# Kernel optimization log

Measured on AMD Instinct MI355X. Metric: run time of the kernel, lower is better.

Reference implementation:

```python
import jax, jax.numpy as jnp
import numpy as np

B, S, D = 2, 1024, 2048
H, HKV, HD = 16, 8, 128
F, E, R = 5632, 8, 16
EPS = 1e-5
SCALE = 2.0  # lora_alpha / r = 32 / 16


def _rope_tables():
    pos = jnp.arange(S, dtype=jnp.float32)
    inv = 1.0 / (10000.0 ** (jnp.arange(0, HD, 2, dtype=jnp.float32) / HD))
    ang = pos[:, None] * inv[None, :]  # [S, HD/2]
    return jnp.cos(ang), jnp.sin(ang)


def setup_inputs() -> dict:
    key = jax.random.key(0)
    ks = jax.random.split(key, 18)
    p = lambda k, shp: jax.random.normal(k, shp, dtype=jnp.float32) * 0.02
    cos, sin = _rope_tables()
    return {
        'data': jax.random.normal(ks[0], (B, S, D), dtype=jnp.float32),
        'mask': jnp.zeros((1, 1, S, S), dtype=jnp.float32),
        'rope_cos': cos,
        'rope_sin': sin,
        'attn_norm_w': jnp.ones((D,), jnp.float32),
        'ffn_norm_w': jnp.ones((D,), jnp.float32),
        'wq': p(ks[1], (D, D)),
        'wk': p(ks[2], (HKV * HD, D)),
        'wv': p(ks[3], (HKV * HD, D)),
        'wo': p(ks[4], (D, D)),
        'gate_w': p(ks[5], (E, D)),
        'w1': p(ks[6], (F, D)),
        'w2': p(ks[7], (D, F)),
        'w3': p(ks[8], (F, D)),
        'w1_a': p(ks[9], (E, R, D)),
        'w1_b': p(ks[10], (E, F, R)),
        'w3_a': p(ks[11], (E, R, D)),
        'w3_b': p(ks[12], (E, F, R)),
        'w2_a': p(ks[13], (E, R, F)),
        'w2_b': p(ks[14], (E, D, R)),
    }


def _rmsnorm(x, w):
    v = jnp.mean(x.astype(jnp.float32) ** 2, axis=-1, keepdims=True)
    return (x * jax.lax.rsqrt(v + EPS)).astype(x.dtype) * w


def _rope(x, cos, sin):
    # x: [B,S,h,HD]; interleaved-pair rotation (llama apply_rotary_emb)
    x1, x2 = x[..., 0::2], x[..., 1::2]
    c, s = cos[None, :, None, :], sin[None, :, None, :]
    o1 = x1 * c - x2 * s
    o2 = x1 * s + x2 * c
    return jnp.stack([o1, o2], axis=-1).reshape(x.shape)


def reference(data, mask, rope_cos, rope_sin, attn_norm_w, ffn_norm_w,
              wq, wk, wv, wo, gate_w, w1, w2, w3,
              w1_a, w1_b, w3_a, w3_b, w2_a, w2_b):
    # ---- attention block ----
    xn = _rmsnorm(data, attn_norm_w)
    q = (xn @ wq.T).reshape(B, S, H, HD)
    k = (xn @ wk.T).reshape(B, S, HKV, HD)
    v = (xn @ wv.T).reshape(B, S, HKV, HD)
    q = _rope(q, rope_cos, rope_sin)
    k = _rope(k, rope_cos, rope_sin)
    k = jnp.repeat(k, H // HKV, axis=2)  # repeat_kv
    v = jnp.repeat(v, H // HKV, axis=2)
    scores = jnp.einsum('bqhd,bkhd->bhqk', q, k) / np.float32(np.sqrt(HD)) + mask
    probs = jax.nn.softmax(scores, axis=-1)
    attn = jnp.einsum('bhqk,bkhd->bqhd', probs, v).reshape(B, S, H * HD)
    data = data + attn @ wo.T
    # ---- MoE block ----
    sn = _rmsnorm(data, ffn_norm_w)
    logits = sn @ gate_w.T  # [B,S,E]
    # NOTE: source uses F.softmax(..., dim=1) -> softmax over SEQ axis, replicated faithfully
    rw = jax.nn.softmax(logits.astype(jnp.float32), axis=1)
    rw, sel = jax.lax.top_k(rw, 2)  # over experts (last axis)
    rw = rw / jnp.sum(rw, axis=-1, keepdims=True)
    c1 = sn @ w1.T  # [B,S,F]
    c3 = sn @ w3.T
    acc = jnp.zeros_like(data)
    for e in range(E):  # dense per-expert loop, as in source
        h1 = c1 + ((sn @ w1_a[e].T) @ w1_b[e].T) * SCALE
        h3 = c3 + ((sn @ w3_a[e].T) @ w3_b[e].T) * SCALE
        sr = jax.nn.silu(h1) * h3
        h = sr @ w2.T + ((sr @ w2_a[e].T) @ w2_b[e].T) * SCALE
        ew = jnp.sum(rw * (sel == e), axis=-1, keepdims=True).astype(h.dtype)
        acc = acc + h * ew
    return data + acc
```

## Files before the change

kernel.cpp:

```cpp
#include <hip/hip_runtime.h>
#include <hip/hip_bf16.h>
#include <stdint.h>

#define DEVI __device__ __forceinline__

typedef __attribute__((ext_vector_type(8))) short short8;
typedef __attribute__((ext_vector_type(4))) short short4b;
typedef __attribute__((ext_vector_type(4))) float f32x4;

constexpr int Bb  = 2, Ss = 1024, Dd = 2048, Hh = 16, HKVv = 8, HDd = 128;
constexpr int Ff  = 5632, Ee = 8, Rr = 16;
constexpr int Tt  = Bb * Ss;
constexpr int M2  = 2 * Tt;
constexpr int NKV = HKVv * HDd;
constexpr int NQKV = Dd + 2 * NKV;

DEVI unsigned short f2bf(float f) {
  union { float f; unsigned u; } x; x.f = f;
  unsigned r = (x.u + 0x7FFFu + ((x.u >> 16) & 1u)) >> 16;
  return (unsigned short)r;
}
DEVI float bf2f(unsigned short h) {
  union { unsigned u; float f; } x; x.u = ((unsigned)h) << 16; return x.f;
}
DEVI float wsum64(float v) {
  #pragma unroll
  for (int d = 1; d < 64; d <<= 1) v += __shfl_xor(v, d, 64);
  return v;
}
DEVI float wsum16(float v) {
  v += __shfl_xor(v, 1, 64); v += __shfl_xor(v, 2, 64);
  v += __shfl_xor(v, 4, 64); v += __shfl_xor(v, 8, 64);
  return v;
}
DEVI float wmax16(float v) {
  v = fmaxf(v, __shfl_xor(v, 1, 64)); v = fmaxf(v, __shfl_xor(v, 2, 64));
  v = fmaxf(v, __shfl_xor(v, 4, 64)); v = fmaxf(v, __shfl_xor(v, 8, 64));
  return v;
}
typedef __attribute__((address_space(1))) void gvoid;
typedef __attribute__((address_space(3))) void lvoid;
DEVI void gl_lds16(const void* g, void* l) {
  __builtin_amdgcn_global_load_lds((gvoid*)g, (lvoid*)l, 16, 0, 0);
}
DEVI unsigned ldsoff(const void* p) {
  return (unsigned)(uintptr_t)(lvoid*)p;
}
DEVI f32x4 mfma16x16(short8 a, short8 b, f32x4 c) {
  return __builtin_amdgcn_mfma_f32_16x16x32_bf16(a, b, c, 0, 0, 0);
}

__global__ __launch_bounds__(256) void cast_w(const float* __restrict__ in,
                                              unsigned short* __restrict__ out, int n) {
  int i = (blockIdx.x * 256 + threadIdx.x) * 8;
  if (i >= n) return;
  const float4* p = (const float4*)(in + i);
  float4 a = p[0], b = p[1];
  float v[8] = {a.x,a.y,a.z,a.w,b.x,b.y,b.z,b.w};
  short8 o;
  #pragma unroll
  for (int j = 0; j < 8; ++j) o[j] = (short)f2bf(v[j]);
  *(short8*)(out + i) = o;
}
__global__ __launch_bounds__(256) void cast_split_w(const float* __restrict__ in,
                                                    unsigned short* __restrict__ oh,
                                                    unsigned short* __restrict__ ol, int n) {
  int i = (blockIdx.x * 256 + threadIdx.x) * 8;
  if (i >= n) return;
  const float4* p = (const float4*)(in + i);
  float4 a = p[0], b = p[1];
  float v[8] = {a.x,a.y,a.z,a.w,b.x,b.y,b.z,b.w};
  short8 h, l;
  #pragma unroll
  for (int j = 0; j < 8; ++j) {
    unsigned short hb = f2bf(v[j]);
    h[j] = (short)hb;
    l[j] = (short)f2bf(v[j] - bf2f(hb));
  }
  *(short8*)(oh + i) = h;
  *(short8*)(ol + i) = l;
}

__global__ __launch_bounds__(256) void rmsnorm_k(const float* __restrict__ x,
                                                 const float* __restrict__ w,
                                                 unsigned short* __restrict__ out) {
  int row = blockIdx.x, tid = threadIdx.x;
  const float* xr = x + (size_t)row * Dd;
  const float4* p4 = (const float4*)(xr + tid * 8);
  float4 a = p4[0], b = p4[1];
  float v[8] = {a.x,a.y,a.z,a.w,b.x,b.y,b.z,b.w};
  float ss = 0.f;
  #pragma unroll
  for (int j = 0; j < 8; ++j) ss += v[j] * v[j];
  ss = wsum64(ss);
  __shared__ float red[4];
  int wv_ = tid >> 6, l = tid & 63;
  if (l == 0) red[wv_] = ss;
  __syncthreads();
  float tot = red[0] + red[1] + red[2] + red[3];
  float rstd = rsqrtf(tot * (1.0f / Dd) + 1e-5f);
  const float* wr = w + tid * 8;
  short8 o;
  #pragma unroll
  for (int j = 0; j < 8; ++j) o[j] = (short)f2bf(v[j] * rstd * wr[j]);
  *(short8*)(out + (size_t)row * Dd + tid * 8) = o;
}

__global__ __launch_bounds__(256) void rmsnorm_split_k(const float* __restrict__ x,
                                                       const float* __restrict__ w,
                                                       unsigned short* __restrict__ outh,
                                                       unsigned short* __restrict__ outl) {
  int row = blockIdx.x, tid = threadIdx.x;
  const float* xr = x + (size_t)row * Dd;
  const float4* p4 = (const float4*)(xr + tid * 8);
  float4 a = p4[0], b = p4[1];
  float v[8] = {a.x,a.y,a.z,a.w,b.x,b.y,b.z,b.w};
  float ss = 0.f;
  #pragma unroll
  for (int j = 0; j < 8; ++j) ss += v[j] * v[j];
  ss = wsum64(ss);
  __shared__ float red[4];
  int wv_ = tid >> 6, l = tid & 63;
  if (l == 0) red[wv_] = ss;
  __syncthreads();
  float tot = red[0] + red[1] + red[2] + red[3];
  float rstd = rsqrtf(tot * (1.0f / Dd) + 1e-5f);
  const float* wr = w + tid * 8;
  short8 oh, ol;
  #pragma unroll
  for (int j = 0; j < 8; ++j) {
    float val = v[j] * rstd * wr[j];
    unsigned short hb = f2bf(val);
    oh[j] = (short)hb;
    ol[j] = (short)f2bf(val - bf2f(hb));
  }
  *(short8*)(outh + (size_t)row * Dd + tid * 8) = oh;
  *(short8*)(outl + (size_t)row * Dd + tid * 8) = ol;
}

template <int MODE>
__global__ __launch_bounds__(256) void gemm_bt64_db(const unsigned short* __restrict__ A,
                                                    const unsigned short* __restrict__ Bw,
                                                    void* __restrict__ Cout,
                                                    int M, int N, int K, int gx) {
  __shared__ __align__(16) unsigned short As[2][128 * 64];
  __shared__ __align__(16) unsigned short Bs[2][128 * 64];
  int tid = threadIdx.x;
  int w = tid >> 6, l = tid & 63;
  int lr = l & 15, lg = l >> 4;
  int cpx = (int)gridDim.x >> 3;
  int bid = blockIdx.x;
  int swz = (bid & 7) * cpx + (bid >> 3);
  int bx = swz % gx, by = swz / gx;
  int m0 = by * 128, n0 = bx * 128;
  int wr = (w >> 1) * 64, wc = (w & 1) * 64;
  f32x4 acc[4][4];
  #pragma unroll
  for (int i = 0; i < 4; ++i)
    #pragma unroll
    for (int j = 0; j < 4; ++j) acc[i][j] = (f32x4){0.f, 0.f, 0.f, 0.f};

  int srow = w * 32 + (l >> 3);
  int schunk = (l & 7) ^ (l >> 3);
  const unsigned short* ga = A  + (size_t)(m0 + srow) * K + schunk * 8;
  const unsigned short* gb = Bw + (size_t)(n0 + srow) * K + schunk * 8;

  auto STAGE = [&](int b, int k0) {
    #pragma unroll
    for (int c = 0; c < 4; ++c) {
      gl_lds16(ga + k0 + (size_t)(c * 8) * K, As[b] + w * 2048 + c * 512);
      gl_lds16(gb + k0 + (size_t)(c * 8) * K, Bs[b] + w * 2048 + c * 512);
    }
  };
  auto COMP = [&](int b) {
    const unsigned short* Ab = As[b];
    const unsigned short* Bb = Bs[b];
    #pragma unroll
    for (int kk = 0; kk < 2; ++kk) {
      short8 af[4], bfr[4];
      #pragma unroll
      for (int i = 0; i < 4; ++i)
        af[i]  = *(const short8*)(Ab + (wr + i * 16 + lr) * 64 + (((kk * 4 + lg) ^ (lr & 7)) * 8));
      #pragma unroll
      for (int j = 0; j < 4; ++j)
        bfr[j] = *(const short8*)(Bb + (wc + j * 16 + lr) * 64 + (((kk * 4 + lg) ^ (lr & 7)) * 8));
      #pragma unroll
      for (int i = 0; i < 4; ++i)
        #pragma unroll
        for (int j = 0; j < 4; ++j) acc[i][j] = mfma16x16(af[i], bfr[j], acc[i][j]);
    }
  };

  int nk = K >> 6;
  STAGE(0, 0);
  __syncthreads();
  int cur = 0;
  for (int kt = 0; kt < nk - 1; ++kt) {
    STAGE(cur ^ 1, (kt + 1) << 6);
    COMP(cur);
    __syncthreads();
    cur ^= 1;
  }
  COMP(cur);

  #pragma unroll
  for (int i = 0; i < 4; ++i)
    #pragma unroll
    for (int j = 0; j < 4; ++j) {
      int m = m0 + wr + i * 16 + lg * 4;
      int n = n0 + wc + j * 16 + lr;
      #pragma unroll
      for (int r = 0; r < 4; ++r) {
        float vv = acc[i][j][r];
        size_t o = (size_t)(m + r) * N + n;
        if (MODE == 0) ((unsigned short*)Cout)[o] = f2bf(vv);
        else           ((float*)Cout)[o] = vv;
      }
    }
}

template <int MODE>
__global__ __launch_bounds__(256) void gemm3_bt(const unsigned short* __restrict__ Ah,
                                                const unsigned short* __restrict__ Al,
                                                const unsigned short* __restrict__ Bh1,
                                                const unsigned short* __restrict__ Bl1,
                                                const unsigned short* __restrict__ Bh2,
                                                const unsigned short* __restrict__ Bl2,
                                                const unsigned short* __restrict__ Bh3,
                                                const unsigned short* __restrict__ Bl3,
                                                int nsplit1, int nsplit2,
                                                void* __restrict__ C0,
                                                const float* __restrict__ resid,
                                                int M, int N, int K, int gx) {
  __shared__ __align__(16) unsigned short Ash[128 * 32];
  __shared__ __align__(16) unsigned short Asl[128 * 32];
  __shared__ __align__(16) unsigned short Bsh[128 * 32];
  __shared__ __align__(16) unsigned short Bsl[128 * 32];
  int tid = threadIdx.x;
  int w = tid >> 6, l = tid & 63;
  int lr = l & 15, lg = l >> 4;
  int cpx = (int)gridDim.x >> 3;
  int bid = blockIdx.x;
  int swz = (bid & 7) * cpx + (bid >> 3);
  int bx = swz % gx, by = swz / gx;
  int m0 = by * 128, n0 = bx * 128;
  int wr = (w >> 1) * 64, wc = (w & 1) * 64;

  const unsigned short* Bh; const unsigned short* Bl; int nb;
  if (n0 < nsplit1)      { Bh = Bh1; Bl = Bl1; nb = n0; }
  else if (n0 < nsplit2) { Bh = Bh2; Bl = Bl2; nb = n0 - nsplit1; }
  else                   { Bh = Bh3; Bl = Bl3; nb = n0 - nsplit2; }

  f32x4 acc[4][4];
  #pragma unroll
  for (int i = 0; i < 4; ++i)
    #pragma unroll
    for (int j = 0; j < 4; ++j) acc[i][j] = (f32x4){0.f, 0.f, 0.f, 0.f};

  int srow = w * 32 + (l >> 2);
  int scol = ((l & 3) ^ ((l >> 3) & 3)) * 8;
  const unsigned short* gah = Ah + (size_t)(m0 + srow) * K + scol;
  const unsigned short* gal = Al + (size_t)(m0 + srow) * K + scol;
  const unsigned short* gbh = Bh + (size_t)(nb + srow) * K + scol;
  const unsigned short* gbl = Bl + (size_t)(nb + srow) * K + scol;
  unsigned short* lAh = Ash + w * 1024;
  unsigned short* lAl = Asl + w * 1024;
  unsigned short* lBh = Bsh + w * 1024;
  unsigned short* lBl = Bsl + w * 1024;

  for (int k0 = 0; k0 < K; k0 += 32) {
    gl_lds16(gah + k0, lAh); gl_lds16(gah + (size_t)16 * K + k0, lAh + 512);
    gl_lds16(gal + k0, lAl); gl_lds16(gal + (size_t)16 * K + k0, lAl + 512);
    gl_lds16(gbh + k0, lBh); gl_lds16(gbh + (size_t)16 * K + k0, lBh + 512);
    gl_lds16(gbl + k0, lBl); gl_lds16(gbl + (size_t)16 * K + k0, lBl + 512);
    __syncthreads();
    int rc = (lg ^ ((lr >> 1) & 3)) * 8;
    short8 afh[4], afl[4], bfh[4], bfl[4];
    #pragma unroll
    for (int i = 0; i < 4; ++i) {
      afh[i] = *(const short8*)(Ash + (wr + i * 16 + lr) * 32 + rc);
      afl[i] = *(const short8*)(Asl + (wr + i * 16 + lr) * 32 + rc);
    }
    #pragma unroll
    for (int j = 0; j < 4; ++j) {
      bfh[j] = *(const short8*)(Bsh + (wc + j * 16 + lr) * 32 + rc);
      bfl[j] = *(const short8*)(Bsl + (wc + j * 16 + lr) * 32 + rc);
    }
    #pragma unroll
    for (int i = 0; i < 4; ++i)
      #pragma unroll
      for (int j = 0; j < 4; ++j) {
        acc[i][j] = mfma16x16(afh[i], bfh[j], acc[i][j]);
        acc[i][j] = mfma16x16(afh[i], bfl[j], acc[i][j]);
        acc[i][j] = mfma16x16(afl[i], bfh[j], acc[i][j]);
      }
    __syncthreads();
  }
  #pragma unroll
  for (int i = 0; i < 4; ++i)
    #pragma unroll
    for (int j = 0; j < 4; ++j) {
      int m = m0 + wr + i * 16 + lg * 4;
      int n = n0 + wc + j * 16 + lr;
      #pragma unroll
      for (int r = 0; r < 4; ++r) {
        float vv = acc[i][j][r];
        size_t o = (size_t)(m + r) * N + n;
        if (MODE == 1) ((float*)C0)[o] = vv;
        else           ((float*)C0)[o] = vv + resid[o];
      }
    }
}

__global__ __launch_bounds__(128) void vsplit_k(const float* __restrict__ qkv,
                                                unsigned short* __restrict__ vh,
                                                unsigned short* __restrict__ vl) {
  int row = blockIdx.x;
  int bas = threadIdx.x * 8;
  const float4* p = (const float4*)(qkv + (size_t)row * NQKV + Dd + NKV + bas);
  float4 a = p[0], b = p[1];
  float v[8] = {a.x,a.y,a.z,a.w,b.x,b.y,b.z,b.w};
  short8 h, l;
  #pragma unroll
  for (int j = 0; j < 8; ++j) {
    unsigned short hb = f2bf(v[j]);
    h[j] = (short)hb;
    l[j] = (short)f2bf(v[j] - bf2f(hb));
  }
  size_t o = (size_t)row * NKV + bas;
  *(short8*)(vh + o) = h;
  *(short8*)(vl + o) = l;
}

__global__ void rope_split_k(const float* __restrict__ x, int xstride,
                             const float* __restrict__ cs, const float* __restrict__ sn,
                             unsigned short* __restrict__ oh, unsigned short* __restrict__ ol,
                             int nh) {
  int row = blockIdx.x;
  int s = row & (Ss - 1);
  int nelem = nh * HDd;
  int bas = threadIdx.x * 8;
  if (bas >= nelem) return;
  const float4* px = (const float4*)(x + (size_t)row * xstride + bas);
  float4 a = px[0], b = px[1];
  float vv[8] = {a.x,a.y,a.z,a.w,b.x,b.y,b.z,b.w};
  int d = bas & (HDd - 1);
  const float* cr = cs + s * 64 + (d >> 1);
  const float* sr = sn + s * 64 + (d >> 1);
  short8 hs, ls;
  #pragma unroll
  for (int p = 0; p < 4; ++p) {
    float x1 = vv[2 * p], x2 = vv[2 * p + 1];
    float c = cr[p], si = sr[p];
    float o1 = x1 * c - x2 * si;
    float o2 = x1 * si + x2 * c;
    unsigned short h1 = f2bf(o1), h2 = f2bf(o2);
    hs[2 * p] = (short)h1;      hs[2 * p + 1] = (short)h2;
    ls[2 * p] = (short)f2bf(o1 - bf2f(h1));
    ls[2 * p + 1] = (short)f2bf(o2 - bf2f(h2));
  }
  size_t o = (size_t)row * nelem + bas;
  *(short8*)(oh + o) = hs;
  *(short8*)(ol + o) = ls;
}

__global__ __launch_bounds__(256) void attn3_k(const unsigned short* __restrict__ qh,
                                               const unsigned short* __restrict__ ql,
                                               const unsigned short* __restrict__ kh,
                                               const unsigned short* __restrict__ kl,
                                               const unsigned short* __restrict__ vh,
                                               const unsigned short* __restrict__ vl,
                                               const float* __restrict__ mask,
                                               unsigned short* __restrict__ aoh,
                                               unsigned short* __restrict__ aol) {
  __shared__ __align__(16) unsigned short Ksh[32 * 128], Ksl[32 * 128];
  __shared__ __align__(16) unsigned short VTh[8 * 528], VTl[8 * 528];
  __shared__ __align__(16) unsigned short Plh[4 * 16 * 40], Pll[4 * 16 * 40];
  int tid = threadIdx.x, w = tid >> 6, l = tid & 63;
  int lr = l & 15, lg = l >> 4;
  int b = blockIdx.y >> 4, h = blockIdx.y & 15, hk = h >> 1;
  int q0 = blockIdx.x * 64 + w * 16;

  short8 qfh[4], qfl[4];
  {
    size_t qoff = ((size_t)((b * Ss + q0 + lr) * Hh + h)) * HDd;
    #pragma unroll
    for (int ds = 0; ds < 4; ++ds) {
      qfh[ds] = *(const short8*)(qh + qoff + ds * 32 + lg * 8);
      qfl[ds] = *(const short8*)(ql + qoff + ds * 32 + lg * 8);
    }
  }

  float mreg[4] = {-1e30f, -1e30f, -1e30f, -1e30f};
  float lreg[4] = {0.f, 0.f, 0.f, 0.f};
  f32x4 oacc[8];
  #pragma unroll
  for (int db = 0; db < 8; ++db) oacc[db] = (f32x4){0.f, 0.f, 0.f, 0.f};

  const float sc = 0.08838834764831845f;
  size_t kvbase = ((size_t)(b * Ss) * HKVv + hk) * HDd;
  const unsigned short* kb_h = kh + kvbase;
  const unsigned short* kb_l = kl + kvbase;
  const unsigned short* vb_h = vh + kvbase;
  const unsigned short* vb_l = vl + kvbase;

  int kc1 = (lr ^ lg) * 8;
  int kc2 = (lr ^ (lg + 4)) * 8;
  int vrow_a = w * 8 + ((l & 7) >> 1);
  int vchunk = ((l >> 3) * 2 + (l & 1)) * 8;
  unsigned short* vh1 = VTh + (2 * w) * 528;
  unsigned short* vh2 = VTh + (2 * w + 1) * 528;
  unsigned short* vl1 = VTl + (2 * w) * 528;
  unsigned short* vl2 = VTl + (2 * w + 1) * 528;
  unsigned vtbh = ldsoff(VTh) + (unsigned)lr * 8u;
  unsigned vtbl = ldsoff(VTl) + (unsigned)lr * 8u;

  for (int kv0 = 0; kv0 < Ss; kv0 += 32) {
    int r1 = kv0 + w * 8 + lg;
    gl_lds16(kb_h + (size_t)r1 * NKV + kc1,       Ksh + w * 1024);
    gl_lds16(kb_h + (size_t)(r1 + 4) * NKV + kc2, Ksh + w * 1024 + 512);
    gl_lds16(kb_l + (size_t)r1 * NKV + kc1,       Ksl + w * 1024);
    gl_lds16(kb_l + (size_t)(r1 + 4) * NKV + kc2, Ksl + w * 1024 + 512);
    int vr0 = kv0 + vrow_a;
    gl_lds16(vb_h + (size_t)vr0 * NKV + vchunk,       vh1);
    gl_lds16(vb_h + (size_t)(vr0 + 4) * NKV + vchunk, vh2);
    gl_lds16(vb_l + (size_t)vr0 * NKV + vchunk,       vl1);
    gl_lds16(vb_l + (size_t)(vr0 + 4) * NKV + vchunk, vl2);
    __syncthreads();

    f32x4 s0 = (f32x4){0.f,0.f,0.f,0.f}, s1 = (f32x4){0.f,0.f,0.f,0.f};
    #pragma unroll
    for (int ds = 0; ds < 4; ++ds) {
      int kcol = ((ds * 4 + lg) ^ (lr & 7)) * 8;
      short8 kh0 = *(const short8*)(Ksh + lr * 128 + kcol);
      short8 kh1 = *(const short8*)(Ksh + (16 + lr) * 128 + kcol);
      short8 kl0 = *(const short8*)(Ksl + lr * 128 + kcol);
      short8 kl1 = *(const short8*)(Ksl + (16 + lr) * 128 + kcol);
      s0 = mfma16x16(qfh[ds], kh0, s0);
      s0 = mfma16x16(qfh[ds], kl0, s0);
      s0 = mfma16x16(qfl[ds], kh0, s0);
      s1 = mfma16x16(qfh[ds], kh1, s1);
      s1 = mfma16x16(qfh[ds], kl1, s1);
      s1 = mfma16x16(qfl[ds], kh1, s1);
    }
    const float* mrow = mask + (size_t)(q0 + lg * 4) * Ss + kv0 + lr;
    #pragma unroll
    for (int r = 0; r < 4; ++r) {
      float a0 = s0[r] * sc + mrow[(size_t)r * Ss];
      float a1 = s1[r] * sc + mrow[(size_t)r * Ss + 16];
      float t = wmax16(fmaxf(a0, a1));
      float mn = fmaxf(mreg[r], t);
      float resc = __expf(mreg[r] - mn);
      mreg[r] = mn;
      float e0 = __expf(a0 - mn), e1 = __expf(a1 - mn);
      float ps = wsum16(e0 + e1);
      lreg[r] = lreg[r] * resc + ps;
      #pragma unroll
      for (int db = 0; db < 8; ++db) oacc[db][r] *= resc;
      unsigned short h0 = f2bf(e0), h1 = f2bf(e1);
      unsigned short* prowh = Plh + (w * 16 + lg * 4 + r) * 40;
      unsigned short* prowl = Pll + (w * 16 + lg * 4 + r) * 40;
      prowh[lr] = h0;            prowh[16 + lr] = h1;
      prowl[lr] = f2bf(e0 - bf2f(h0));
      prowl[16 + lr] = f2bf(e1 - bf2f(h1));
    }
    asm volatile("" ::: "memory");
    short8 pfh = *(const short8*)(Plh + (w * 16 + lr) * 40 + lg * 8);
    short8 pfl = *(const short8*)(Pll + (w * 16 + lr) * 40 + lg * 8);

    short4b v4[16];
    #pragma unroll
    for (int db = 0; db < 8; ++db) {
      #pragma unroll
      for (int t = 0; t < 2; ++t) {
        unsigned off = vtbh + (unsigned)((lg * 2 + t) * 1056 + db * 128);
        asm volatile("ds_read_b64_tr_b16 %0, %1" : "=v"(v4[db * 2 + t]) : "v"(off));
      }
    }
    asm volatile("s_waitcnt lgkmcnt(0)" ::: "memory");
    __builtin_amdgcn_sched_barrier(0);
    #pragma unroll
    for (int db = 0; db < 8; ++db) {
      short8 vf;
      vf[0] = v4[db*2][0]; vf[1] = v4[db*2][1]; vf[2] = v4[db*2][2]; vf[3] = v4[db*2][3];
      vf[4] = v4[db*2+1][0]; vf[5] = v4[db*2+1][1]; vf[6] = v4[db*2+1][2]; vf[7] = v4[db*2+1][3];
      oacc[db] = mfma16x16(pfh, vf, oacc[db]);
      oacc[db] = mfma16x16(pfl, vf, oacc[db]);
    }
    #pragma unroll
    for (int db = 0; db < 8; ++db) {
      #pragma unroll
      for (int t = 0; t < 2; ++t) {
        unsigned off = vtbl + (unsigned)((lg * 2 + t) * 1056 + db * 128);
        asm volatile("ds_read_b64_tr_b16 %0, %1" : "=v"(v4[db * 2 + t]) : "v"(off));
      }
    }
    asm volatile("s_waitcnt lgkmcnt(0)" ::: "memory");
    __builtin_amdgcn_sched_barrier(0);
    #pragma unroll
    for (int db = 0; db < 8; ++db) {
      short8 vf;
      vf[0] = v4[db*2][0]; vf[1] = v4[db*2][1]; vf[2] = v4[db*2][2]; vf[3] = v4[db*2][3];
      vf[4] = v4[db*2+1][0]; vf[5] = v4[db*2+1][1]; vf[6] = v4[db*2+1][2]; vf[7] = v4[db*2+1][3];
      oacc[db] = mfma16x16(pfh, vf, oacc[db]);
    }
    __syncthreads();
  }
  float inv[4];
  #pragma unroll
  for (int r = 0; r < 4; ++r) inv[r] = 1.0f / lreg[r];
  size_t obase = ((size_t)((b * Ss + q0 + lg * 4) * Hh + h)) * HDd + lr;
  #pragma unroll
  for (int db = 0; db < 8; ++db)
    #pragma unroll
    for (int r = 0; r < 4; ++r) {
      float val = oacc[db][r] * inv[r];
      unsigned short hb = f2bf(val);
      size_t o = obase + (size_t)r * Hh * HDd + db * 16;
      aoh[o] = hb;
      aol[o] = f2bf(val - bf2f(hb));
    }
}

__global__ __launch_bounds__(256) void router_logits(const float* __restrict__ x2,
                                                     const float* __restrict__ fnw,
                                                     const float* __restrict__ gw,
                                                     float* __restrict__ logits) {
  int wid = (blockIdx.x * 256 + threadIdx.x) >> 6;
  int l = threadIdx.x & 63;
  if (wid >= Tt) return;
  const float* row = x2 + (size_t)wid * Dd;
  float xs[32]; float ss = 0.f;
  #pragma unroll
  for (int c = 0; c < 32; ++c) { float t = row[c * 64 + l]; xs[c] = t; ss += t * t; }
  ss = wsum64(ss);
  float rstd = rsqrtf(ss * (1.0f / Dd) + 1e-5f);
  #pragma unroll
  for (int c = 0; c < 32; ++c) xs[c] *= rstd * fnw[c * 64 + l];
  for (int e = 0; e < 8; ++e) {
    float a = 0.f;
    #pragma unroll
    for (int c = 0; c < 32; ++c) a += xs[c] * gw[(size_t)e * Dd + c * 64 + l];
    a = wsum64(a);
    if (l == 0) logits[wid * 8 + e] = a;
  }
}
__global__ __launch_bounds__(256) void router_colstats(const float* __restrict__ logits,
                                                       float* __restrict__ mz) {
  int b = blockIdx.x >> 3, e = blockIdx.x & 7;
  int tid = threadIdx.x, wv_ = tid >> 6, l = tid & 63;
  __shared__ float red[4];
  float mx = -1e30f;
  for (int s = tid; s < Ss; s += 256) mx = fmaxf(mx, logits[(size_t)(b * Ss + s) * 8 + e]);
  #pragma unroll
  for (int d = 1; d < 64; d <<= 1) mx = fmaxf(mx, __shfl_xor(mx, d, 64));
  if (l == 0) red[wv_] = mx;
  __syncthreads();
  mx = fmaxf(fmaxf(red[0], red[1]), fmaxf(red[2], red[3]));
  __syncthreads();
  float z = 0.f;
  for (int s = tid; s < Ss; s += 256) z += expf(logits[(size_t)(b * Ss + s) * 8 + e] - mx);
  z = wsum64(z);
  if (l == 0) red[wv_] = z;
  __syncthreads();
  if (tid == 0) {
    mz[(b * 8 + e) * 2] = mx;
    mz[(b * 8 + e) * 2 + 1] = red[0] + red[1] + red[2] + red[3];
  }
}
__global__ __launch_bounds__(256) void router_select(const float* __restrict__ logits,
                                                     const float* __restrict__ mz,
                                                     int* __restrict__ sel,
                                                     float* __restrict__ ewt) {
  int t = blockIdx.x * 256 + threadIdx.x;
  if (t >= Tt) return;
  int b = t >> 10;
  float rw[8];
  #pragma unroll
  for (int e = 0; e < 8; ++e)
    rw[e] = expf(logits[(size_t)t * 8 + e] - mz[(b * 8 + e) * 2]) / mz[(b * 8 + e) * 2 + 1];
  int i0 = 0; float b0 = rw[0];
  #pragma unroll
  for (int e = 1; e < 8; ++e) if (rw[e] > b0) { b0 = rw[e]; i0 = e; }
  int i1 = -1; float b1 = -1.f;
  #pragma unroll
  for (int e = 0; e < 8; ++e) if (e != i0 && rw[e] > b1) { b1 = rw[e]; i1 = e; }
  float s = b0 + b1;
  sel[2 * t] = i0; sel[2 * t + 1] = i1;
  ewt[2 * t] = b0 / s; ewt[2 * t + 1] = b1 / s;
}
__global__ void zero_cnt_k(int* cnt) { if (threadIdx.x < 8) cnt[threadIdx.x] = 0; }
__global__ void gather_k(const int* __restrict__ sel, int* cnt, int* list) {
  int i = blockIdx.x * 256 + threadIdx.x;
  if (i >= M2) return;
  int e = sel[i];
  int pos = atomicAdd(cnt + e, 1);
  list[e * Tt + pos] = i;
}

__global__ __launch_bounds__(256) void lora_up_k(const unsigned short* __restrict__ snb,
                                                 const int* __restrict__ sel,
                                                 const float* __restrict__ w1a,
                                                 const float* __restrict__ w3a,
                                                 float* __restrict__ t1, float* __restrict__ t3) {
  int i = (blockIdx.x * 256 + threadIdx.x) >> 6;
  int l = threadIdx.x & 63;
  if (i >= M2) return;
  int t = i >> 1, e = sel[i];
  const unsigned short* row = snb + (size_t)t * Dd;
  const float* wa1 = w1a + (size_t)e * Rr * Dd;
  const float* wa3 = w3a + (size_t)e * Rr * Dd;
  float a1[16], a3[16];
  #pragma unroll
  for (int r = 0; r < 16; ++r) { a1[r] = 0.f; a3[r] = 0.f; }
  for (int c0 = 0; c0 < 32; c0 += 8) {
    float xs[8];
    #pragma unroll
    for (int c = 0; c < 8; ++c) xs[c] = bf2f(row[(c0 + c) * 64 + l]);
    #pragma unroll
    for (int r = 0; r < 16; ++r) {
      float s1 = a1[r], s3 = a3[r];
      #pragma unroll
      for (int c = 0; c < 8; ++c) {
        s1 += xs[c] * wa1[(size_t)r * Dd + (c0 + c) * 64 + l];
        s3 += xs[c] * wa3[(size_t)r * Dd + (c0 + c) * 64 + l];
      }
      a1[r] = s1; a3[r] = s3;
    }
  }
  #pragma unroll
  for (int r = 0; r < 16; ++r) { a1[r] = wsum64(a1[r]); a3[r] = wsum64(a3[r]); }
  if (l == 0) {
    #pragma unroll
    for (int r = 0; r < 16; ++r) { t1[i * 16 + r] = a1[r]; t3[i * 16 + r] = a3[r]; }
  }
}

__global__ __launch_bounds__(256) void expert_sr_k(const unsigned short* __restrict__ c1,
                                                   const unsigned short* __restrict__ c3,
                                                   const float* __restrict__ t1,
                                                   const float* __restrict__ t3,
                                                   const float* __restrict__ w1b,
                                                   const float* __restrict__ w3b,
                                                   const int* __restrict__ cnt,
                                                   const int* __restrict__ list,
                                                   unsigned short* __restrict__ sr) {
  int e = blockIdx.y;
  int f = blockIdx.x * 256 + threadIdx.x;
  __shared__ float W1[16 * 256], W3[16 * 256];
  #pragma unroll
  for (int r = 0; r < 16; ++r) {
    W1[r * 256 + threadIdx.x] = 2.0f * w1b[((size_t)e * Ff + f) * 16 + r];
    W3[r * 256 + threadIdx.x] = 2.0f * w3b[((size_t)e * Ff + f) * 16 + r];
  }
  __syncthreads();
  int n = cnt[e];
  int chunk = (n + 3) >> 2;
  int pbeg = blockIdx.z * chunk;
  int pend = min(n, pbeg + chunk);
  for (int p = pbeg; p < pend; ++p) {
    int i = list[e * Tt + p];
    int t = i >> 1;
    const float* u1 = t1 + (size_t)i * 16;
    const float* u3 = t3 + (size_t)i * 16;
    float l1 = 0.f, l3 = 0.f;
    #pragma unroll
    for (int r = 0; r < 16; ++r) {
      l1 += u1[r] * W1[r * 256 + threadIdx.x];
      l3 += u3[r] * W3[r * 256 + threadIdx.x];
    }
    float h1 = bf2f(c1[(size_t)t * Ff + f]) + l1;
    float h3 = bf2f(c3[(size_t)t * Ff + f]) + l3;
    float sv = (h1 / (1.f + __expf(-h1))) * h3;
    sr[(size_t)i * Ff + f] = f2bf(sv);
  }
}

__global__ __launch_bounds__(256) void lora_down_k(const unsigned short* __restrict__ sr,
                                                   const int* __restrict__ sel,
                                                   const float* __restrict__ w2a,
                                                   float* __restrict__ t2) {
  int i = (blockIdx.x * 256 + threadIdx.x) >> 6;
  int l = threadIdx.x & 63;
  if (i >= M2) return;
  int e = sel[i];
  const unsigned short* row = sr + (size_t)i * Ff;
  const float* wa = w2a + (size_t)e * Rr * Ff;
  float acc[16];
  #pragma unroll
  for (int r = 0; r < 16; ++r) acc[r] = 0.f;
  for (int c0 = 0; c0 < 88; c0 += 11) {
    float xs[11];
    #pragma unroll
    for (int c = 0; c < 11; ++c) xs[c] = bf2f(row[(c0 + c) * 64 + l]);
    #pragma unroll
    for (int r = 0; r < 16; ++r) {
      float a = acc[r];
      #pragma unroll
      for (int c = 0; c < 11; ++c) a += xs[c] * wa[(size_t)r * Ff + (c0 + c) * 64 + l];
      acc[r] = a;
    }
  }
  #pragma unroll
  for (int r = 0; r < 16; ++r) acc[r] = wsum64(acc[r]);
  if (l == 0) {
    #pragma unroll
    for (int r = 0; r < 16; ++r) t2[i * 16 + r] = acc[r];
  }
}

__global__ __launch_bounds__(256) void combine_k(const float* __restrict__ hb,
                                                 const float* __restrict__ t2,
                                                 const int* __restrict__ sel,
                                                 const float* __restrict__ ewt,
                                                 const float* __restrict__ w2b,
                                                 float* __restrict__ out) {
  int t = blockIdx.x;
  int d0 = threadIdx.x * 8;
  int e0 = sel[2 * t], e1 = sel[2 * t + 1];
  float a0 = ewt[2 * t], a1 = ewt[2 * t + 1];
  float uu0[16], uu1[16];
  const float* u0 = t2 + (size_t)(2 * t) * 16;
  const float* u1 = t2 + (size_t)(2 * t + 1) * 16;
  #pragma unroll
  for (int r = 0; r < 16; ++r) { uu0[r] = u0[r]; uu1[r] = u1[r]; }
  const float* wb0 = w2b + (size_t)e0 * Dd * 16;
  const float* wb1 = w2b + (size_t)e1 * Dd * 16;
  const float* h0 = hb + (size_t)(2 * t) * Dd;
  const float* h1 = hb + (size_t)(2 * t + 1) * Dd;
  float* orow = out + (size_t)t * Dd;
  #pragma unroll
  for (int dd = 0; dd < 8; ++dd) {
    int d = d0 + dd;
    float l0 = 0.f, l1v = 0.f;
    #pragma unroll
    for (int r = 0; r < 16; ++r) {
      l0  += uu0[r] * wb0[(size_t)d * 16 + r];
      l1v += uu1[r] * wb1[(size_t)d * 16 + r];
    }
    orow[d] += a0 * (h0[d] + 2.f * l0) + a1 * (h1[d] + 2.f * l1v);
  }
}

extern "C" void kernel_launch(void* const* d_in, const int* in_sizes, int n_in,
                              void* d_out, int out_size, void* d_ws, size_t ws_size,
                              hipStream_t stream) {
  const float* data  = (const float*)d_in[0];
  const float* mask  = (const float*)d_in[1];
  const float* ropec = (const float*)d_in[2];
  const float* ropes = (const float*)d_in[3];
  const float* anw   = (const float*)d_in[4];
  const float* fnw   = (const float*)d_in[5];
  const float* wq_f  = (const float*)d_in[6];
  const float* wk_f  = (const float*)d_in[7];
  const float* wv_f  = (const float*)d_in[8];
  const float* wo_f  = (const float*)d_in[9];
  const float* gate  = (const float*)d_in[10];
  const float* w1_f  = (const float*)d_in[11];
  const float* w2_f  = (const float*)d_in[12];
  const float* w3_f  = (const float*)d_in[13];
  const float* w1a   = (const float*)d_in[14];
  const float* w1bl  = (const float*)d_in[15];
  const float* w3a   = (const float*)d_in[16];
  const float* w3bl  = (const float*)d_in[17];
  const float* w2a   = (const float*)d_in[18];
  const float* w2bl  = (const float*)d_in[19];
  float* out = (float*)d_out;

  char* base = (char*)d_ws;
  size_t off = 0;
  auto take = [&](size_t bytes) -> char* {
    char* r = base + off;
    off += (bytes + 255) & ~(size_t)255;
    return r;
  };
  unsigned short* wqh = (unsigned short*)take((size_t)Dd * Dd * 2);
  unsigned short* wql = (unsigned short*)take((size_t)Dd * Dd * 2);
  unsigned short* wkh = (unsigned short*)take((size_t)NKV * Dd * 2);
  unsigned short* wkl = (unsigned short*)take((size_t)NKV * Dd * 2);
  unsigned short* wvh = (unsigned short*)take((size_t)NKV * Dd * 2);
  unsigned short* wvl = (unsigned short*)take((size_t)NKV * Dd * 2);
  unsigned short* woh = (unsigned short*)take((size_t)Dd * Dd * 2);
  unsigned short* wol = (unsigned short*)take((size_t)Dd * Dd * 2);
  unsigned short* w1bf = (unsigned short*)take((size_t)Ff * Dd * 2);
  unsigned short* w2bf = (unsigned short*)take((size_t)Dd * Ff * 2);
  unsigned short* w3bf = (unsigned short*)take((size_t)Ff * Dd * 2);
  unsigned short* xh = (unsigned short*)take((size_t)Tt * Dd * 2);
  unsigned short* xl = (unsigned short*)take((size_t)Tt * Dd * 2);
  unsigned short* qhB = (unsigned short*)take((size_t)Tt * Dd * 2);
  unsigned short* qlB = (unsigned short*)take((size_t)Tt * Dd * 2);
  unsigned short* khB = (unsigned short*)take((size_t)Tt * NKV * 2);
  unsigned short* klB = (unsigned short*)take((size_t)Tt * NKV * 2);
  unsigned short* vhB = (unsigned short*)take((size_t)Tt * NKV * 2);
  unsigned short* vlB = (unsigned short*)take((size_t)Tt * NKV * 2);
  unsigned short* srb = (unsigned short*)take((size_t)M2 * Ff * 2);
  float* hb = (float*)take((size_t)M2 * Dd * 4);
  float* t1b = (float*)take((size_t)M2 * 16 * 4);
  float* t3b = (float*)take((size_t)M2 * 16 * 4);
  float* t2b = (float*)take((size_t)M2 * 16 * 4);
  int*   selb = (int*)take((size_t)M2 * 4);
  float* ewtb = (float*)take((size_t)M2 * 4);
  float* logitsb = (float*)take((size_t)Tt * 8 * 4);
  float* mzb = (float*)take((size_t)16 * 2 * 4);
  int*   cntb = (int*)take(8 * 4);
  int*   listb = (int*)take((size_t)8 * Tt * 4);
  if (off > ws_size) return;

  float* qkv = (float*)hb;
  unsigned short* aoh = xh;
  unsigned short* aol = xl;
  unsigned short* snb = qhB;
  unsigned short* c1b = qlB;
  unsigned short* c3b = wqh;

  cast_split_w<<<2048, 256, 0, stream>>>(wq_f, wqh, wql, Dd * Dd);
  cast_split_w<<<1024, 256, 0, stream>>>(wk_f, wkh, wkl, NKV * Dd);
  cast_split_w<<<1024, 256, 0, stream>>>(wv_f, wvh, wvl, NKV * Dd);
  cast_split_w<<<2048, 256, 0, stream>>>(wo_f, woh, wol, Dd * Dd);
  cast_w<<<5632, 256, 0, stream>>>(w1_f, w1bf, Ff * Dd);
  cast_w<<<5632, 256, 0, stream>>>(w2_f, w2bf, Dd * Ff);
  cast_w<<<5632, 256, 0, stream>>>(w3_f, w3bf, Ff * Dd);

  rmsnorm_split_k<<<Tt, 256, 0, stream>>>(data, anw, xh, xl);
  gemm3_bt<1><<<512, 256, 0, stream>>>(xh, xl, wqh, wql, wkh, wkl, wvh, wvl,
                                       Dd, Dd + NKV, qkv, nullptr, Tt, NQKV, Dd, 32);
  vsplit_k<<<Tt, 128, 0, stream>>>(qkv, vhB, vlB);
  rope_split_k<<<Tt, 256, 0, stream>>>(qkv, NQKV, ropec, ropes, qhB, qlB, Hh);
  rope_split_k<<<Tt, 128, 0, stream>>>(qkv + Dd, NQKV, ropec, ropes, khB, klB, HKVv);
  attn3_k<<<dim3(16, 32), 256, 0, stream>>>(qhB, qlB, khB, klB, vhB, vlB, mask, aoh, aol);
  gemm3_bt<2><<<256, 256, 0, stream>>>(aoh, aol, woh, wol, woh, wol, woh, wol,
                                       Dd, Dd, d_out, data, Tt, Dd, Dd, 16);

  rmsnorm_k<<<Tt, 256, 0, stream>>>(out, fnw, snb);
  router_logits<<<512, 256, 0, stream>>>(out, fnw, gate, logitsb);
  router_colstats<<<16, 256, 0, stream>>>(logitsb, mzb);
  router_select<<<8, 256, 0, stream>>>(logitsb, mzb, selb, ewtb);
  zero_cnt_k<<<1, 64, 0, stream>>>(cntb);
  gather_k<<<16, 256, 0, stream>>>(selb, cntb, listb);
  gemm_bt64_db<0><<<704, 256, 0, stream>>>(snb, w1bf, c1b, Tt, Ff, Dd, 44);
  gemm_bt64_db<0><<<704, 256, 0, stream>>>(snb, w3bf, c3b, Tt, Ff, Dd, 44);
  lora_up_k<<<1024, 256, 0, stream>>>(snb, selb, w1a, w3a, t1b, t3b);
  expert_sr_k<<<dim3(22, 8, 4), 256, 0, stream>>>(c1b, c3b, t1b, t3b, w1bl, w3bl, cntb, listb, srb);
  lora_down_k<<<1024, 256, 0, stream>>>(srb, selb, w2a, t2b);
  gemm_bt64_db<1><<<512, 256, 0, stream>>>(srb, w2bf, hb, M2, Dd, Ff, 16);
  combine_k<<<Tt, 256, 0, stream>>>(hb, t2b, selb, ewtb, w2bl, out);
}
```

Before: 1.031 ms.

## Merge w1/w3 GEMMs, split-K the w2 GEMM, single-buffer LDS

The w1 and w3 weights are cast into one concatenated matrix, so c1 and c3 come from a single GEMM launch over 2F output columns. The w2 down-projection GEMM is split into two K halves writing separate fp32 partial buffers, which combine_k sums, doubling the block count. The GEMM kernel drops LDS double-buffering for a single buffer with two barriers per K step, halving shared memory and possibly raising occupancy at the cost of load/compute overlap. expert_sr_k splits its token range across twice as many z-blocks.

After: 1.024 ms. No clear change (-0.8%).

```diff
diff --git a/kernel.cpp b/kernel.cpp
--- a/kernel.cpp
+++ b/kernel.cpp
@@ -14,6 +14,7 @@
 constexpr int M2  = 2 * Tt;
 constexpr int NKV = HKVv * HDd;
 constexpr int NQKV = Dd + 2 * NKV;
+constexpr int F2  = 2 * Ff;
 
 DEVI unsigned short f2bf(float f) {
   union { float f; unsigned u; } x; x.f = f;
@@ -139,12 +140,13 @@
 }
 
 template <int MODE>
-__global__ __launch_bounds__(256) void gemm_bt64_db(const unsigned short* __restrict__ A,
+__global__ __launch_bounds__(256) void gemm_bt64_v2(const unsigned short* __restrict__ A,
                                                     const unsigned short* __restrict__ Bw,
-                                                    void* __restrict__ Cout,
-                                                    int M, int N, int K, int gx) {
-  __shared__ __align__(16) unsigned short As[2][128 * 64];
-  __shared__ __align__(16) unsigned short Bs[2][128 * 64];
+                                                    void* __restrict__ C0,
+                                                    void* __restrict__ C1,
+                                                    int M, int N, int Kext, int ld, int gx) {
+  __shared__ __align__(16) unsigned short As[128 * 64];
+  __shared__ __align__(16) unsigned short Bs[128 * 64];
   int tid = threadIdx.x;
   int w = tid >> 6, l = tid & 63;
   int lr = l & 15, lg = l >> 4;
@@ -152,7 +154,11 @@
   int bid = blockIdx.x;
   int swz = (bid & 7) * cpx + (bid >> 3);
   int bx = swz % gx, by = swz / gx;
+  int mtiles = M >> 7;
+  int ks = 0;
+  if (by >= mtiles) { ks = 1; by -= mtiles; }
   int m0 = by * 128, n0 = bx * 128;
+  int koff = ks * Kext;
   int wr = (w >> 1) * 64, wc = (w & 1) * 64;
   f32x4 acc[4][4];
   #pragma unroll
@@ -162,47 +168,35 @@
 
   int srow = w * 32 + (l >> 3);
   int schunk = (l & 7) ^ (l >> 3);
-  const unsigned short* ga = A  + (size_t)(m0 + srow) * K + schunk * 8;
-  const unsigned short* gb = Bw + (size_t)(n0 + srow) * K + schunk * 8;
-
-  auto STAGE = [&](int b, int k0) {
+  const unsigned short* ga = A  + (size_t)(m0 + srow) * ld + koff + schunk * 8;
+  const unsigned short* gb = Bw + (size_t)(n0 + srow) * ld + koff + schunk * 8;
+  unsigned short* lA = As + w * 2048;
+  unsigned short* lB = Bs + w * 2048;
+
+  for (int k0 = 0; k0 < Kext; k0 += 64) {
     #pragma unroll
     for (int c = 0; c < 4; ++c) {
-      gl_lds16(ga + k0 + (size_t)(c * 8) * K, As[b] + w * 2048 + c * 512);
-      gl_lds16(gb + k0 + (size_t)(c * 8) * K, Bs[b] + w * 2048 + c * 512);
-    }
-  };
-  auto COMP = [&](int b) {
-    const unsigned short* Ab = As[b];
-    const unsigned short* Bb = Bs[b];
+      gl_lds16(ga + k0 + (size_t)(c * 8) * ld, lA + c * 512);
+      gl_lds16(gb + k0 + (size_t)(c * 8) * ld, lB + c * 512);
+    }
+    __syncthreads();
     #pragma unroll
     for (int kk = 0; kk < 2; ++kk) {
       short8 af[4], bfr[4];
       #pragma unroll
       for (int i = 0; i < 4; ++i)
-        af[i]  = *(const short8*)(Ab + (wr + i * 16 + lr) * 64 + (((kk * 4 + lg) ^ (lr & 7)) * 8));
+        af[i]  = *(const short8*)(As + (wr + i * 16 + lr) * 64 + (((kk * 4 + lg) ^ (lr & 7)) * 8));
       #pragma unroll
       for (int j = 0; j < 4; ++j)
-        bfr[j] = *(const short8*)(Bb + (wc + j * 16 + lr) * 64 + (((kk * 4 + lg) ^ (lr & 7)) * 8));
+        bfr[j] = *(const short8*)(Bs + (wc + j * 16 + lr) * 64 + (((kk * 4 + lg) ^ (lr & 7)) * 8));
       #pragma unroll
       for (int i = 0; i < 4; ++i)
         #pragma unroll
         for (int j = 0; j < 4; ++j) acc[i][j] = mfma16x16(af[i], bfr[j], acc[i][j]);
     }
-  };
-
-  int nk = K >> 6;
-  STAGE(0, 0);
-  __syncthreads();
-  int cur = 0;
-  for (int kt = 0; kt < nk - 1; ++kt) {
-    STAGE(cur ^ 1, (kt + 1) << 6);
-    COMP(cur);
     __syncthreads();
-    cur ^= 1;
-  }
-  COMP(cur);
-
+  }
+  float* Cf = (float*)(ks ? C1 : C0);
   #pragma unroll
   for (int i = 0; i < 4; ++i)
     #pragma unroll
@@ -213,8 +207,8 @@
       for (int r = 0; r < 4; ++r) {
         float vv = acc[i][j][r];
         size_t o = (size_t)(m + r) * N + n;
-        if (MODE == 0) ((unsigned short*)Cout)[o] = f2bf(vv);
-        else           ((float*)Cout)[o] = vv;
+        if (MODE == 0) ((unsigned short*)C0)[o] = f2bf(vv);
+        else           Cf[o] = vv;
       }
     }
 }
@@ -636,8 +630,7 @@
   }
 }
 
-__global__ __launch_bounds__(256) void expert_sr_k(const unsigned short* __restrict__ c1,
-                                                   const unsigned short* __restrict__ c3,
+__global__ __launch_bounds__(256) void expert_sr_k(const unsigned short* __restrict__ c13,
                                                    const float* __restrict__ t1,
                                                    const float* __restrict__ t3,
                                                    const float* __restrict__ w1b,
@@ -655,7 +648,7 @@
   }
   __syncthreads();
   int n = cnt[e];
-  int chunk = (n + 3) >> 2;
+  int chunk = (n + 7) >> 3;
   int pbeg = blockIdx.z * chunk;
   int pend = min(n, pbeg + chunk);
   for (int p = pbeg; p < pend; ++p) {
@@ -669,8 +662,8 @@
       l1 += u1[r] * W1[r * 256 + threadIdx.x];
       l3 += u3[r] * W3[r * 256 + threadIdx.x];
     }
-    float h1 = bf2f(c1[(size_t)t * Ff + f]) + l1;
-    float h3 = bf2f(c3[(size_t)t * Ff + f]) + l3;
+    float h1 = bf2f(c13[(size_t)t * F2 + f]) + l1;
+    float h3 = bf2f(c13[(size_t)t * F2 + Ff + f]) + l3;
     float sv = (h1 / (1.f + __expf(-h1))) * h3;
     sr[(size_t)i * Ff + f] = f2bf(sv);
   }
@@ -709,7 +702,8 @@
   }
 }
 
-__global__ __launch_bounds__(256) void combine_k(const float* __restrict__ hb,
+__global__ __launch_bounds__(256) void combine_k(const float* __restrict__ hb0,
+                                                 const float* __restrict__ hb1,
                                                  const float* __restrict__ t2,
                                                  const int* __restrict__ sel,
                                                  const float* __restrict__ ewt,
@@ -726,8 +720,7 @@
   for (int r = 0; r < 16; ++r) { uu0[r] = u0[r]; uu1[r] = u1[r]; }
   const float* wb0 = w2b + (size_t)e0 * Dd * 16;
   const float* wb1 = w2b + (size_t)e1 * Dd * 16;
-  const float* h0 = hb + (size_t)(2 * t) * Dd;
-  const float* h1 = hb + (size_t)(2 * t + 1) * Dd;
+  size_t r0 = (size_t)(2 * t) * Dd, r1 = (size_t)(2 * t + 1) * Dd;
   float* orow = out + (size_t)t * Dd;
   #pragma unroll
   for (int dd = 0; dd < 8; ++dd) {
@@ -738,7 +731,9 @@
       l0  += uu0[r] * wb0[(size_t)d * 16 + r];
       l1v += uu1[r] * wb1[(size_t)d * 16 + r];
     }
-    orow[d] += a0 * (h0[d] + 2.f * l0) + a1 * (h1[d] + 2.f * l1v);
+    float h0 = hb0[r0 + d] + hb1[r0 + d];
+    float h1 = hb0[r1 + d] + hb1[r1 + d];
+    orow[d] += a0 * (h0 + 2.f * l0) + a1 * (h1 + 2.f * l1v);
   }
 }
 
@@ -782,9 +777,8 @@
   unsigned short* wvl = (unsigned short*)take((size_t)NKV * Dd * 2);
   unsigned short* woh = (unsigned short*)take((size_t)Dd * Dd * 2);
   unsigned short* wol = (unsigned short*)take((size_t)Dd * Dd * 2);
-  unsigned short* w1bf = (unsigned short*)take((size_t)Ff * Dd * 2);
-  unsigned short* w2bf = (unsigned short*)take((size_t)Dd * Ff * 2);
-  unsigned short* w3bf = (unsigned short*)take((size_t)Ff * Dd * 2);
+  unsigned short* w13bf = (unsigned short*)take((size_t)F2 * Dd * 2);
+  unsigned short* w2bf  = (unsigned short*)take((size_t)Dd * Ff * 2);
   unsigned short* xh = (unsigned short*)take((size_t)Tt * Dd * 2);
   unsigned short* xl = (unsigned short*)take((size_t)Tt * Dd * 2);
   unsigned short* qhB = (unsigned short*)take((size_t)Tt * Dd * 2);
@@ -810,16 +804,16 @@
   unsigned short* aoh = xh;
   unsigned short* aol = xl;
   unsigned short* snb = qhB;
-  unsigned short* c1b = qlB;
-  unsigned short* c3b = wqh;
+  unsigned short* c13b = wqh;
+  float* hb1 = (float*)xh;
 
   cast_split_w<<<2048, 256, 0, stream>>>(wq_f, wqh, wql, Dd * Dd);
   cast_split_w<<<1024, 256, 0, stream>>>(wk_f, wkh, wkl, NKV * Dd);
   cast_split_w<<<1024, 256, 0, stream>>>(wv_f, wvh, wvl, NKV * Dd);
   cast_split_w<<<2048, 256, 0, stream>>>(wo_f, woh, wol, Dd * Dd);
-  cast_w<<<5632, 256, 0, stream>>>(w1_f, w1bf, Ff * Dd);
+  cast_w<<<5632, 256, 0, stream>>>(w1_f, w13bf, Ff * Dd);
+  cast_w<<<5632, 256, 0, stream>>>(w3_f, w13bf + (size_t)Ff * Dd, Ff * Dd);
   cast_w<<<5632, 256, 0, stream>>>(w2_f, w2bf, Dd * Ff);
-  cast_w<<<5632, 256, 0, stream>>>(w3_f, w3bf, Ff * Dd);
 
   rmsnorm_split_k<<<Tt, 256, 0, stream>>>(data, anw, xh, xl);
   gemm3_bt<1><<<512, 256, 0, stream>>>(xh, xl, wqh, wql, wkh, wkl, wvh, wvl,
@@ -837,11 +831,10 @@
   router_select<<<8, 256, 0, stream>>>(logitsb, mzb, selb, ewtb);
   zero_cnt_k<<<1, 64, 0, stream>>>(cntb);
   gather_k<<<16, 256, 0, stream>>>(selb, cntb, listb);
-  gemm_bt64_db<0><<<704, 256, 0, stream>>>(snb, w1bf, c1b, Tt, Ff, Dd, 44);
-  gemm_bt64_db<0><<<704, 256, 0, stream>>>(snb, w3bf, c3b, Tt, Ff, Dd, 44);
+  gemm_bt64_v2<0><<<1408, 256, 0, stream>>>(snb, w13bf, c13b, nullptr, Tt, F2, Dd, Dd, 88);
   lora_up_k<<<1024, 256, 0, stream>>>(snb, selb, w1a, w3a, t1b, t3b);
-  expert_sr_k<<<dim3(22, 8, 4), 256, 0, stream>>>(c1b, c3b, t1b, t3b, w1bl, w3bl, cntb, listb, srb);
+  expert_sr_k<<<dim3(22, 8, 8), 256, 0, stream>>>(c13b, t1b, t3b, w1bl, w3bl, cntb, listb, srb);
   lora_down_k<<<1024, 256, 0, stream>>>(srb, selb, w2a, t2b);
-  gemm_bt64_db<1><<<512, 256, 0, stream>>>(srb, w2bf, hb, M2, Dd, Ff, 16);
-  combine_k<<<Tt, 256, 0, stream>>>(hb, t2b, selb, ewtb, w2bl, out);
-}
+  gemm_bt64_v2<1><<<1024, 256, 0, stream>>>(srb, w2bf, hb, hb1, M2, Dd, Ff / 2, Ff, 16);
+  combine_k<<<Tt, 256, 0, stream>>>(hb, hb1, t2b, selb, ewtb, w2bl, out);
+}
```
